# Kernel tuning notes

Hardware: AMD Instinct MI355X
Metric: run time of the kernel (lower is better)

## Reference

```python
import jax, jax.numpy as jnp
import numpy as np

N = 100_000        # nodes
E_HALF = 1_600_000 # undirected edges; symmetrized -> 3.2M directed
N_IN, N_HEMB, N_HGCN, N_OUT = 128, 32, 32, 1


def setup_inputs() -> dict:
    key = jax.random.key(0)
    ks = jax.random.split(key, 8)
    x = jax.random.normal(ks[0], (N, N_IN), dtype=jnp.float32)
    t = jax.random.uniform(ks[1], (N,), dtype=jnp.float32)
    # symmetric edge list (A = A^T), matching the typical undirected-graph usage
    src = jax.random.randint(ks[2], (E_HALF,), 0, N)
    dst = jax.random.randint(ks[3], (E_HALF,), 0, N)
    row = jnp.concatenate([src, dst]).astype(jnp.int32)
    col = jnp.concatenate([dst, src]).astype(jnp.int32)
    s = 0.05
    W_emb = jax.random.normal(ks[4], (N_IN, N_HEMB), jnp.float32) * s
    b_emb = jnp.zeros((N_HEMB,), jnp.float32)
    W_gcn = jax.random.normal(ks[5], (N_HEMB, N_HGCN), jnp.float32) * s
    b_gcn = jnp.zeros((N_HGCN,), jnp.float32)
    W1 = jax.random.normal(ks[6], (N_HGCN + 2, N_HEMB), jnp.float32) * s
    b1 = jnp.zeros((N_HEMB,), jnp.float32)
    W2 = jax.random.normal(ks[7], (N_HEMB, N_OUT), jnp.float32) * s
    b2 = jnp.zeros((N_OUT,), jnp.float32)
    return dict(x=x, t=t, row=row, col=col,
                W_emb=W_emb, b_emb=b_emb, W_gcn=W_gcn, b_gcn=b_gcn,
                W1=W1, b1=b1, W2=W2, b2=b2)


def reference(x, t, row, col, W_emb, b_emb, W_gcn, b_gcn, W1, b1, W2, b2):
    n = x.shape[0]
    h = jax.nn.relu(x @ W_emb + b_emb)                        # [N, Hemb]
    # per-edge attention score via gather + dot
    att = jnp.einsum('eh,eh->e', h[row], h[col])              # [E]
    att = jnp.exp(att - att.max())                            # global-max stabilized exp
    # per-node softmax denominator (segment sum over neighbors) + eps
    deno = jax.ops.segment_sum(att, row, num_segments=n) + 1e-8
    att = att / deno[row]                                     # normalized edge attention
    # exposure z: attention-weighted neighbor treatments
    z = jax.ops.segment_sum(att * t[col], row, num_segments=n)  # [N]
    # GCNConv (unit edge values: set_value() is non-inplace so adj_t stays valueless;
    # PyG then fills 1s, adds self loops, symmetric D^-1/2 norm)
    deg = jax.ops.segment_sum(jnp.ones(row.shape, jnp.float32), col, num_segments=n) + 1.0
    dis = jax.lax.rsqrt(deg)                                  # [N], deg >= 1
    hw = h @ W_gcn                                            # [N, Hgcn]
    msg = dis[row][:, None] * hw[row]                         # [E, Hgcn]
    agg = jax.ops.segment_sum(msg, col, num_segments=n)       # [N, Hgcn]
    gcn = dis[:, None] * agg + (dis * dis)[:, None] * hw + b_gcn
    rep = h + jax.nn.relu(gcn)                                # residual node rep
    feats = jnp.concatenate([rep, t[:, None], z[:, None]], axis=1)  # [N, Hgcn+2]
    out = jax.nn.relu(feats @ W1 + b1) @ W2 + b2              # [N, 1]
    return out, rep, z
```

## Files before the change

kernel.cpp:

```cpp
#include <hip/hip_runtime.h>
#include <hip/hip_bf16.h>
#include <hip/hip_fp16.h>

static constexpr int HN = 32;
static constexpr int NIN = 128;
static constexpr int CH1 = 8192;
static constexpr int CAP2 = 16384;

__device__ __forceinline__ float bf2f(unsigned short u) {
    union { unsigned int i; float f; } v;
    v.i = ((unsigned int)u) << 16;
    return v.f;
}
__device__ __forceinline__ float ldf(const void* p, size_t i, int isbf) {
    return isbf ? bf2f(((const unsigned short*)p)[i]) : ((const float*)p)[i];
}
__device__ __forceinline__ unsigned int pack2h(float a, float b) {
    unsigned short ua = __half_as_ushort(__float2half_rn(a));
    unsigned short ub = __half_as_ushort(__float2half_rn(b));
    return (unsigned int)ua | ((unsigned int)ub << 16);
}
__device__ __forceinline__ float2 up2(unsigned int u) {
    __half2 h2;
    *reinterpret_cast<unsigned int*>(&h2) = u;
    return __half22float2(h2);
}

__global__ void detect_kernel(const unsigned int* __restrict__ xw,
                              int* __restrict__ flag)
{
    int lane = threadIdx.x;
    int hits = 0;
    #pragma unroll
    for (int k = 0; k < 2; ++k) {
        unsigned int w = xw[lane + 64 * k];
        float a = bf2f((unsigned short)(w & 0xFFFFu));
        float aa = fabsf(a);
        if (a == 0.0f || (aa >= 0.000244140625f && aa <= 32.0f)) hits++;
    }
    #pragma unroll
    for (int m = 32; m; m >>= 1) hits += __shfl_xor(hits, m, 64);
    if (lane == 0) flag[0] = (hits >= 64) ? 1 : 0;
}

__global__ __launch_bounds__(256) void embed1_kernel(
    const void* __restrict__ x,
    const void* __restrict__ Wemb,
    const void* __restrict__ bemb,
    const int* __restrict__ flagp,
    float* __restrict__ h, int N)
{
    __shared__ float We[NIN * HN];
    __shared__ float be[HN];
    __shared__ float xs[32][NIN];
    const int tid = threadIdx.x;
    const int isbf = flagp[0];

    for (int i = tid; i < NIN * HN; i += 256) We[i] = ldf(Wemb, i, isbf);
    if (tid < HN) be[tid] = ldf(bemb, tid, isbf);

    const int n0 = blockIdx.x * 32;
    if (isbf) {
        const ushort4* x4 = (const ushort4*)((const unsigned short*)x + (size_t)n0 * NIN);
        for (int i = tid; i < 32 * (NIN / 4); i += 256) {
            ushort4 u = x4[i];
            int base = i * 4, n = base >> 7, k = base & (NIN - 1);
            xs[n][k] = bf2f(u.x); xs[n][k + 1] = bf2f(u.y);
            xs[n][k + 2] = bf2f(u.z); xs[n][k + 3] = bf2f(u.w);
        }
    } else {
        const float4* x4 = (const float4*)((const float*)x + (size_t)n0 * NIN);
        for (int i = tid; i < 32 * (NIN / 4); i += 256) {
            float4 u = x4[i];
            int base = i * 4, n = base >> 7, k = base & (NIN - 1);
            xs[n][k] = u.x; xs[n][k + 1] = u.y;
            xs[n][k + 2] = u.z; xs[n][k + 3] = u.w;
        }
    }
    __syncthreads();

    const int f = tid & 31, ns = tid >> 5;
    float a0 = be[f], a1 = be[f], a2 = be[f], a3 = be[f];
    #pragma unroll 8
    for (int k = 0; k < NIN; ++k) {
        float w = We[k * HN + f];
        a0 += xs[ns +  0][k] * w;
        a1 += xs[ns +  8][k] * w;
        a2 += xs[ns + 16][k] * w;
        a3 += xs[ns + 24][k] * w;
    }
    if (n0 + ns      < N) h[(size_t)(n0 + ns     ) * HN + f] = fmaxf(a0, 0.f);
    if (n0 + ns +  8 < N) h[(size_t)(n0 + ns +  8) * HN + f] = fmaxf(a1, 0.f);
    if (n0 + ns + 16 < N) h[(size_t)(n0 + ns + 16) * HN + f] = fmaxf(a2, 0.f);
    if (n0 + ns + 24 < N) h[(size_t)(n0 + ns + 24) * HN + f] = fmaxf(a3, 0.f);
}

__global__ __launch_bounds__(512) void bhist_kernel(
    const int* __restrict__ col, int* __restrict__ bucket_cnt, int E, int B)
{
    __shared__ int hist[512];
    const int t = threadIdx.x;
    const int e0 = blockIdx.x * CH1;
    for (int i = t; i < B; i += 512) hist[i] = 0;
    __syncthreads();
    #pragma unroll
    for (int k = 0; k < CH1 / 512; ++k) {
        int e = e0 + k * 512 + t;
        if (e < E) atomicAdd(&hist[col[e] >> 8], 1);
    }
    __syncthreads();
    for (int i = t; i < B; i += 512)
        if (hist[i]) atomicAdd(&bucket_cnt[i], hist[i]);
}

__global__ __launch_bounds__(512) void bscan_kernel(
    const int* __restrict__ bucket_cnt, int* __restrict__ bucket_base,
    int* __restrict__ bucket_cursor, int B, int E)
{
    __shared__ int sc[512];
    __shared__ int orig[512];
    const int t = threadIdx.x;
    int v0 = (t < B) ? bucket_cnt[t] : 0;
    sc[t] = v0; orig[t] = v0;
    __syncthreads();
    for (int o = 1; o < 512; o <<= 1) {
        int v = (t >= o) ? sc[t - o] : 0;
        __syncthreads();
        sc[t] += v;
        __syncthreads();
    }
    if (t < B) {
        int ex = sc[t] - orig[t];
        bucket_base[t] = ex;
        bucket_cursor[t] = ex;
    }
    if (t == 0) bucket_base[B] = E;
}

__global__ __launch_bounds__(512) void phase1_kernel(
    const int* __restrict__ row, const int* __restrict__ col,
    int* __restrict__ bucket_cursor, int* __restrict__ bucketed, int E, int B)
{
    __shared__ int hist[512];
    __shared__ int sc[512];
    __shared__ int cnt[512];
    __shared__ int gbase[512];
    __shared__ int word[CH1];
    __shared__ int dst[CH1];
    const int t = threadIdx.x;
    const int e0 = blockIdx.x * CH1;
    const int M = (E - e0 < CH1) ? (E - e0) : CH1;

    for (int i = t; i < B; i += 512) { hist[i] = 0; cnt[i] = 0; }
    __syncthreads();
    #pragma unroll
    for (int k = 0; k < CH1 / 512; ++k) {
        int e = e0 + k * 512 + t;
        if (e < E) atomicAdd(&hist[col[e] >> 8], 1);
    }
    __syncthreads();
    sc[t] = (t < B) ? hist[t] : 0;
    __syncthreads();
    for (int o = 1; o < 512; o <<= 1) {
        int v = (t >= o) ? sc[t - o] : 0;
        __syncthreads();
        sc[t] += v;
        __syncthreads();
    }
    if (t < B && hist[t])
        gbase[t] = atomicAdd(&bucket_cursor[t], hist[t]);
    __syncthreads();
    #pragma unroll
    for (int k = 0; k < CH1 / 512; ++k) {
        int e = e0 + k * 512 + t;
        if (e < E) {
            int c = col[e], r = row[e];
            int b = c >> 8;
            int lr = atomicAdd(&cnt[b], 1);
            int p = sc[b] - hist[b] + lr;
            word[p] = (r << 8) | (c & 255);
            dst[p] = gbase[b] + lr;
        }
    }
    __syncthreads();
    for (int i = t; i < M; i += 512)
        bucketed[dst[i]] = word[i];
}

__global__ __launch_bounds__(256) void phase2a_kernel(
    const int* __restrict__ bucketed, const int* __restrict__ bucket_base,
    int* __restrict__ count, int N)
{
    __shared__ int cnt[256];
    const int t = threadIdx.x, b = blockIdx.x;
    cnt[t] = 0;
    __syncthreads();
    const int s0 = bucket_base[b], s1 = bucket_base[b + 1];
    for (int i = s0 + t; i < s1; i += 256)
        atomicAdd(&cnt[bucketed[i] & 255], 1);
    __syncthreads();
    int node = (b << 8) + t;
    if (node < N) count[node] = cnt[t];
}

__global__ __launch_bounds__(256) void scan1_kernel(
    const int* __restrict__ count, int* __restrict__ bsum, int N)
{
    __shared__ int s[256];
    const int t = threadIdx.x, b = blockIdx.x;
    int base = b * 2048 + t * 8, sum = 0;
    #pragma unroll
    for (int k = 0; k < 8; ++k) { int i = base + k; if (i < N) sum += count[i]; }
    s[t] = sum; __syncthreads();
    for (int o = 128; o; o >>= 1) { if (t < o) s[t] += s[t + o]; __syncthreads(); }
    if (t == 0) bsum[b] = s[0];
}

__global__ void scan2_kernel(int* __restrict__ bsum, int nsb,
                             int* __restrict__ rowptr, int N, int E)
{
    if (threadIdx.x == 0 && blockIdx.x == 0) {
        int acc = 0;
        for (int i = 0; i < nsb; ++i) { int v = bsum[i]; bsum[i] = acc; acc += v; }
        rowptr[N] = E;
    }
}

__global__ __launch_bounds__(256) void scan3_kernel(
    int* __restrict__ countcur, const int* __restrict__ bsum,
    int* __restrict__ rowptr, int N)
{
    __shared__ int s[256];
    const int t = threadIdx.x, b = blockIdx.x;
    int base = b * 2048 + t * 8;
    int c[8]; int sum = 0;
    #pragma unroll
    for (int k = 0; k < 8; ++k) {
        int i = base + k;
        c[k] = (i < N) ? countcur[i] : 0;
        sum += c[k];
    }
    s[t] = sum; __syncthreads();
    for (int o = 1; o < 256; o <<= 1) {
        int v = (t >= o) ? s[t - o] : 0;
        __syncthreads();
        s[t] += v;
        __syncthreads();
    }
    int acc = bsum[b] + ((t == 0) ? 0 : s[t - 1]);
    #pragma unroll
    for (int k = 0; k < 8; ++k) {
        int i = base + k;
        if (i < N) { rowptr[i] = acc; countcur[i] = acc; acc += c[k]; }
    }
}

__global__ __launch_bounds__(256) void phase2b_kernel(
    const int* __restrict__ bucketed, const int* __restrict__ bucket_base,
    const int* __restrict__ rowptr, int* __restrict__ cursor,
    int* __restrict__ csr_src, int N)
{
    __shared__ int stage[CAP2];
    __shared__ int rps[257];
    __shared__ int cnt[256];
    const int t = threadIdx.x, b = blockIdx.x;
    const int s0 = bucket_base[b], s1 = bucket_base[b + 1];
    const int segsz = s1 - s0;
    const int node0 = b << 8;
    const int nodes = (N - node0 < 256) ? (N - node0) : 256;
    if (t <= nodes) rps[t] = rowptr[node0 + t];
    cnt[t] = 0;
    __syncthreads();
    if (segsz <= CAP2) {
        for (int i = s0 + t; i < s1; i += 256) {
            int w = bucketed[i];
            int lc = w & 255;
            int off = rps[lc] - s0 + atomicAdd(&cnt[lc], 1);
            stage[off] = w >> 8;
        }
        __syncthreads();
        for (int i = t; i < segsz; i += 256) csr_src[s0 + i] = stage[i];
    } else {
        for (int i = s0 + t; i < s1; i += 256) {
            int w = bucketed[i];
            int pos = atomicAdd(&cursor[node0 + (w & 255)], 1);
            csr_src[pos] = w >> 8;
        }
    }
}

__global__ __launch_bounds__(256) void embed2_kernel(
    const float* __restrict__ h, const void* __restrict__ Wgcn,
    const int* __restrict__ rowptr, const int* __restrict__ flagp,
    uint4* __restrict__ packed, int N)
{
    __shared__ float Wg[HN * HN];
    __shared__ float hs[32][HN + 1];
    __shared__ float ws[32][HN + 1];
    const int tid = threadIdx.x;
    const int isbf = flagp[0];
    for (int i = tid; i < HN * HN; i += 256) Wg[i] = ldf(Wgcn, i, isbf);
    const int n0 = blockIdx.x * 32;
    for (int i = tid; i < 32 * HN; i += 256) {
        int n = i >> 5, f = i & 31;
        hs[n][f] = (n0 + n < N) ? h[(size_t)(n0 + n) * HN + f] : 0.f;
    }
    __syncthreads();
    const int f = tid & 31, ns = tid >> 5;
    #pragma unroll
    for (int g = 0; g < 4; ++g) {
        int n = ns + 8 * g, v = n0 + n;
        float acc = 0.f;
        #pragma unroll
        for (int k = 0; k < HN; ++k) acc += hs[n][k] * Wg[k * HN + f];
        float dis = (v < N) ? rsqrtf((float)(rowptr[v + 1] - rowptr[v]) + 1.0f) : 0.f;
        ws[n][f] = dis * acc;
    }
    __syncthreads();
    const int n = tid >> 3, jj = tid & 7, v = n0 + n;
    if (v < N) {
        uint4 w;
        w.x = pack2h(hs[n][4 * jj + 0], hs[n][4 * jj + 1]);
        w.y = pack2h(hs[n][4 * jj + 2], hs[n][4 * jj + 3]);
        w.z = pack2h(ws[n][4 * jj + 0], ws[n][4 * jj + 1]);
        w.w = pack2h(ws[n][4 * jj + 2], ws[n][4 * jj + 3]);
        packed[(size_t)v * 8 + jj] = w;
    }
}

__global__ __launch_bounds__(256) void passB_kernel(
    const float* __restrict__ h, const uint4* __restrict__ packed,
    const int* __restrict__ csr_src, const int* __restrict__ rowptr,
    const void* __restrict__ t, const void* __restrict__ bgcn,
    const int* __restrict__ flagp,
    float* __restrict__ outr, float* __restrict__ outz,
    float* __restrict__ out0_ml, float* __restrict__ denout, int N)
{
    const int tid = threadIdx.x;
    const int lane = tid & 31;
    const int sub = lane >> 3;
    const int j = lane & 7;
    const int v = blockIdx.x * 8 + (tid >> 5);
    if (v >= N) return;
    const int isbf = flagp[0];

    const float4* h4 = (const float4*)h;
    float4 hv = h4[(size_t)v * 8 + j];
    uint4 sw = packed[(size_t)v * 8 + j];
    float2 wsv0 = up2(sw.z), wsv1 = up2(sw.w);
    const int s = rowptr[v], e2 = rowptr[v + 1];

    float m = -1e30f, den = 0.f, num = 0.f;
    float ax = 0.f, ay = 0.f, az = 0.f, aw = 0.f;
    int i = s + sub;
    for (; i + 4 < e2; i += 8) {
        int r0 = csr_src[i];
        int r1 = csr_src[i + 4];
        uint4 w0 = packed[(size_t)r0 * 8 + j];
        uint4 w1 = packed[(size_t)r1 * 8 + j];
        float tr0 = ldf(t, r0, isbf);
        float tr1 = ldf(t, r1, isbf);
        float2 h00 = up2(w0.x), h01 = up2(w0.y);
        float2 h10 = up2(w1.x), h11 = up2(w1.y);
        float p0 = hv.x * h00.x + hv.y * h00.y + hv.z * h01.x + hv.w * h01.y;
        float p1 = hv.x * h10.x + hv.y * h10.y + hv.z * h11.x + hv.w * h11.y;
        p0 += __shfl_xor(p0, 1, 32);
        p0 += __shfl_xor(p0, 2, 32);
        p0 += __shfl_xor(p0, 4, 32);
        p1 += __shfl_xor(p1, 1, 32);
        p1 += __shfl_xor(p1, 2, 32);
        p1 += __shfl_xor(p1, 4, 32);
        float2 a00 = up2(w0.z), a01 = up2(w0.w);
        float2 a10 = up2(w1.z), a11 = up2(w1.w);
        ax += a00.x + a10.x; ay += a00.y + a10.y;
        az += a01.x + a11.x; aw += a01.y + a11.y;
        float mn = fmaxf(m, fmaxf(p0, p1));
        float corr = __expf(m - mn);
        float e0 = __expf(p0 - mn), e1 = __expf(p1 - mn);
        den = den * corr + e0 + e1;
        num = num * corr + e0 * tr0 + e1 * tr1;
        m = mn;
    }
    if (i < e2) {
        int r0 = csr_src[i];
        uint4 w0 = packed[(size_t)r0 * 8 + j];
        float tr0 = ldf(t, r0, isbf);
        float2 h00 = up2(w0.x), h01 = up2(w0.y);
        float p0 = hv.x * h00.x + hv.y * h00.y + hv.z * h01.x + hv.w * h01.y;
        p0 += __shfl_xor(p0, 1, 32);
        p0 += __shfl_xor(p0, 2, 32);
        p0 += __shfl_xor(p0, 4, 32);
        float2 a00 = up2(w0.z), a01 = up2(w0.w);
        ax += a00.x; ay += a00.y; az += a01.x; aw += a01.y;
        float mn = fmaxf(m, p0);
        float corr = __expf(m - mn);
        float e0 = __expf(p0 - mn);
        den = den * corr + e0;
        num = num * corr + e0 * tr0;
        m = mn;
    }
    #pragma unroll
    for (int o = 8; o <= 16; o <<= 1) {
        float mo = __shfl_xor(m, o, 32);
        float dno = __shfl_xor(den, o, 32);
        float nmo = __shfl_xor(num, o, 32);
        float mn = fmaxf(m, mo);
        float ca = __expf(m - mn), cb = __expf(mo - mn);
        den = den * ca + dno * cb;
        num = num * ca + nmo * cb;
        m = mn;
        ax += __shfl_xor(ax, o, 32);
        ay += __shfl_xor(ay, o, 32);
        az += __shfl_xor(az, o, 32);
        aw += __shfl_xor(aw, o, 32);
    }

    float dv = rsqrtf((float)(e2 - s) + 1.0f);
    float4 rep;
    rep.x = hv.x + fmaxf(dv * (ax + wsv0.x) + ldf(bgcn, 4 * j + 0, isbf), 0.f);
    rep.y = hv.y + fmaxf(dv * (ay + wsv0.y) + ldf(bgcn, 4 * j + 1, isbf), 0.f);
    rep.z = hv.z + fmaxf(dv * (az + wsv1.x) + ldf(bgcn, 4 * j + 2, isbf), 0.f);
    rep.w = hv.w + fmaxf(dv * (aw + wsv1.y) + ldf(bgcn, 4 * j + 3, isbf), 0.f);
    if (sub == 0)
        ((float4*)outr)[(size_t)v * 8 + j] = rep;
    if (lane == 0) {
        outz[v]    = num / fmaxf(den, 1e-37f);
        out0_ml[v] = m;
        denout[v]  = den;
    }
}

__global__ __launch_bounds__(256) void amax1_kernel(
    const float* __restrict__ ml, float* __restrict__ bmax2, int N)
{
    float m = -INFINITY;
    for (int i = blockIdx.x * 256 + threadIdx.x; i < N; i += 256 * 256)
        m = fmaxf(m, ml[i]);
    #pragma unroll
    for (int s = 32; s; s >>= 1) m = fmaxf(m, __shfl_xor(m, s, 64));
    __shared__ float sm[4];
    if ((threadIdx.x & 63) == 0) sm[threadIdx.x >> 6] = m;
    __syncthreads();
    if (threadIdx.x == 0)
        bmax2[blockIdx.x] = fmaxf(fmaxf(sm[0], sm[1]), fmaxf(sm[2], sm[3]));
}
__global__ __launch_bounds__(256) void amax2_kernel(
    const float* __restrict__ bmax2, float* __restrict__ amax)
{
    float m = bmax2[threadIdx.x];
    #pragma unroll
    for (int s = 32; s; s >>= 1) m = fmaxf(m, __shfl_xor(m, s, 64));
    __shared__ float sm[4];
    if ((threadIdx.x & 63) == 0) sm[threadIdx.x >> 6] = m;
    __syncthreads();
    if (threadIdx.x == 0) amax[0] = fmaxf(fmaxf(sm[0], sm[1]), fmaxf(sm[2], sm[3]));
}

__global__ __launch_bounds__(256) void final_kernel(
    const float* __restrict__ rep_in,
    const void* __restrict__ t, const int* __restrict__ flagp,
    const float* __restrict__ amax, const float* __restrict__ denarr,
    const void* __restrict__ W1, const void* __restrict__ b1,
    const void* __restrict__ W2, const void* __restrict__ b2,
    float* __restrict__ out0, float* __restrict__ outz, int N)
{
    __shared__ float W1s[34 * HN];
    __shared__ float b1s[HN], W2s[HN];
    __shared__ float b2s;
    const int tid = threadIdx.x;
    const int isbf = flagp[0];
    for (int i = tid; i < 34 * HN; i += 256) W1s[i] = ldf(W1, i, isbf);
    if (tid < HN) {
        b1s[tid] = ldf(b1, tid, isbf);
        W2s[tid] = ldf(W2, tid, isbf);
    }
    if (tid == 0) b2s = ldf(b2, 0, isbf);
    __syncthreads();

    const int lane = tid & 31;
    const int v = blockIdx.x * 8 + (tid >> 5);
    if (v >= N) return;

    float rep = rep_in[(size_t)v * HN + lane];
    float ml  = out0[v];
    float den = denarr[v];
    float zh  = outz[v];
    float am  = amax[0];
    float term = (1e-8f / den) * expf(am - ml);
    float z = zh / (1.0f + term);
    float tv = ldf(t, v, isbf);

    float acc = b1s[lane] + tv * W1s[32 * HN + lane] + z * W1s[33 * HN + lane];
    #pragma unroll
    for (int k = 0; k < HN; ++k)
        acc += __shfl(rep, k, 32) * W1s[k * HN + lane];
    float f1 = fmaxf(acc, 0.f);
    float o = f1 * W2s[lane];
    #pragma unroll
    for (int m = 16; m; m >>= 1) o += __shfl_xor(o, m, 32);

    if (lane == 0) {
        out0[v] = o + b2s;
        outz[v] = z;
    }
}

extern "C" void kernel_launch(void* const* d_in, const int* in_sizes, int n_in,
                              void* d_out, int out_size, void* d_ws, size_t ws_size,
                              hipStream_t stream)
{
    const int N = out_size / 34;
    const int E = in_sizes[2];

    const void* x    = d_in[0];
    const void* t    = d_in[1];
    const int* row   = (const int*)d_in[2];
    const int* col   = (const int*)d_in[3];
    const void* Wemb = d_in[4];
    const void* bemb = d_in[5];
    const void* Wgcn = d_in[6];
    const void* bgcn = d_in[7];
    const void* W1   = d_in[8];
    const void* b1   = d_in[9];
    const void* W2   = d_in[10];
    const void* b2   = d_in[11];

    const int B   = (N + 255) >> 8;
    const int nsb = (N + 2047) / 2048;
    const int NB1 = (E + CH1 - 1) / CH1;

    char* wsb = (char*)d_ws;
    size_t off = 0;
    float* h        = (float*)(wsb + off); off += (size_t)N * HN * 4;
    size_t hwbytes  = (size_t)N * HN * 4;
    if ((size_t)E * 4 > hwbytes) hwbytes = (size_t)E * 4;
    char*  hwreg    = wsb + off;           off += hwbytes;
    int*   csr_src  = (int*)(wsb + off);   off += (size_t)E * 4;
    int*   rowptr   = (int*)(wsb + off);   off += (size_t)(N + 1) * 4;
    int*   count    = (int*)(wsb + off);   off += (size_t)N * 4;
    int*   bucket_cnt    = (int*)(wsb + off); off += (size_t)B * 4;
    int*   bucket_base   = (int*)(wsb + off); off += (size_t)(B + 1) * 4;
    int*   bucket_cursor = (int*)(wsb + off); off += (size_t)B * 4;
    float* bmax2    = (float*)(wsb + off); off += 256 * 4;
    int*   bsum     = (int*)(wsb + off);   off += (size_t)nsb * 4;
    float* amax     = (float*)(wsb + off); off += 4;
    int*   flag     = (int*)(wsb + off);   off += 4;

    int*   bucketed = (int*)hwreg;
    uint4* packed   = (uint4*)hwreg;

    hipMemsetAsync(bucket_cnt, 0, (size_t)B * 4, stream);

    detect_kernel<<<1, 64, 0, stream>>>((const unsigned int*)x, flag);
    embed1_kernel<<<(N + 31) / 32, 256, 0, stream>>>(x, Wemb, bemb, flag, h, N);

    bhist_kernel<<<NB1, 512, 0, stream>>>(col, bucket_cnt, E, B);
    bscan_kernel<<<1, 512, 0, stream>>>(bucket_cnt, bucket_base,
                                        bucket_cursor, B, E);
    phase1_kernel<<<NB1, 512, 0, stream>>>(row, col, bucket_cursor,
                                           bucketed, E, B);
    phase2a_kernel<<<B, 256, 0, stream>>>(bucketed, bucket_base, count, N);
    scan1_kernel<<<nsb, 256, 0, stream>>>(count, bsum, N);
    scan2_kernel<<<1, 64, 0, stream>>>(bsum, nsb, rowptr, N, E);
    scan3_kernel<<<nsb, 256, 0, stream>>>(count, bsum, rowptr, N);
    phase2b_kernel<<<B, 256, 0, stream>>>(bucketed, bucket_base, rowptr,
                                          count, csr_src, N);
    embed2_kernel<<<(N + 31) / 32, 256, 0, stream>>>(h, Wgcn, rowptr, flag,
                                                     packed, N);

    float* outp = (float*)d_out;
    float* out0 = outp;
    float* outr = outp + N;
    float* outz = outp + (size_t)N * 33;
    float* den  = (float*)count;

    passB_kernel<<<(N + 7) / 8, 256, 0, stream>>>(
        h, packed, csr_src, rowptr, t, bgcn, flag, outr, outz, out0, den, N);
    amax1_kernel<<<256, 256, 0, stream>>>(out0, bmax2, N);
    amax2_kernel<<<1, 256, 0, stream>>>(bmax2, amax);
    final_kernel<<<(N + 7) / 8, 256, 0, stream>>>(
        outr, t, flag, amax, den, W1, b1, W2, b2, out0, outz, N);
}
```

Before: 357.2 us.

## Build CSR from global per-node degree count, dropping bucket histogram passes

```diff
diff --git a/kernel.cpp b/kernel.cpp
--- a/kernel.cpp
+++ b/kernel.cpp
@@ -4,8 +4,9 @@
 
 static constexpr int HN = 32;
 static constexpr int NIN = 128;
-static constexpr int CH1 = 8192;
+static constexpr int CH1 = 4096;
 static constexpr int CAP2 = 16384;
+static constexpr float LOG2E = 1.4426950408889634f;
 
 __device__ __forceinline__ float bf2f(unsigned short u) {
     union { unsigned int i; float f; } v;
@@ -95,46 +96,12 @@
     if (n0 + ns + 24 < N) h[(size_t)(n0 + ns + 24) * HN + f] = fmaxf(a3, 0.f);
 }
 
-__global__ __launch_bounds__(512) void bhist_kernel(
-    const int* __restrict__ col, int* __restrict__ bucket_cnt, int E, int B)
-{
-    __shared__ int hist[512];
-    const int t = threadIdx.x;
-    const int e0 = blockIdx.x * CH1;
-    for (int i = t; i < B; i += 512) hist[i] = 0;
-    __syncthreads();
-    #pragma unroll
-    for (int k = 0; k < CH1 / 512; ++k) {
-        int e = e0 + k * 512 + t;
-        if (e < E) atomicAdd(&hist[col[e] >> 8], 1);
-    }
-    __syncthreads();
-    for (int i = t; i < B; i += 512)
-        if (hist[i]) atomicAdd(&bucket_cnt[i], hist[i]);
-}
-
-__global__ __launch_bounds__(512) void bscan_kernel(
-    const int* __restrict__ bucket_cnt, int* __restrict__ bucket_base,
-    int* __restrict__ bucket_cursor, int B, int E)
-{
-    __shared__ int sc[512];
-    __shared__ int orig[512];
-    const int t = threadIdx.x;
-    int v0 = (t < B) ? bucket_cnt[t] : 0;
-    sc[t] = v0; orig[t] = v0;
-    __syncthreads();
-    for (int o = 1; o < 512; o <<= 1) {
-        int v = (t >= o) ? sc[t - o] : 0;
-        __syncthreads();
-        sc[t] += v;
-        __syncthreads();
-    }
-    if (t < B) {
-        int ex = sc[t] - orig[t];
-        bucket_base[t] = ex;
-        bucket_cursor[t] = ex;
-    }
-    if (t == 0) bucket_base[B] = E;
+__global__ __launch_bounds__(256) void degcnt_kernel(
+    const int* __restrict__ col, int* __restrict__ count, int E)
+{
+    const int stride = gridDim.x * 256;
+    for (int i = blockIdx.x * 256 + threadIdx.x; i < E; i += stride)
+        atomicAdd(&count[col[i]], 1);
 }
 
 __global__ __launch_bounds__(512) void phase1_kernel(
@@ -187,22 +154,6 @@
         bucketed[dst[i]] = word[i];
 }
 
-__global__ __launch_bounds__(256) void phase2a_kernel(
-    const int* __restrict__ bucketed, const int* __restrict__ bucket_base,
-    int* __restrict__ count, int N)
-{
-    __shared__ int cnt[256];
-    const int t = threadIdx.x, b = blockIdx.x;
-    cnt[t] = 0;
-    __syncthreads();
-    const int s0 = bucket_base[b], s1 = bucket_base[b + 1];
-    for (int i = s0 + t; i < s1; i += 256)
-        atomicAdd(&cnt[bucketed[i] & 255], 1);
-    __syncthreads();
-    int node = (b << 8) + t;
-    if (node < N) count[node] = cnt[t];
-}
-
 __global__ __launch_bounds__(256) void scan1_kernel(
     const int* __restrict__ count, int* __restrict__ bsum, int N)
 {
@@ -219,16 +170,26 @@
 __global__ void scan2_kernel(int* __restrict__ bsum, int nsb,
                              int* __restrict__ rowptr, int N, int E)
 {
-    if (threadIdx.x == 0 && blockIdx.x == 0) {
+    const int lane = threadIdx.x;
+    if (nsb <= 64) {
+        int v = (lane < nsb) ? bsum[lane] : 0;
+        int s = v;
+        #pragma unroll
+        for (int o = 1; o < 64; o <<= 1) {
+            int u = __shfl_up(s, o, 64);
+            if (lane >= o) s += u;
+        }
+        if (lane < nsb) bsum[lane] = s - v;
+    } else if (lane == 0) {
         int acc = 0;
         for (int i = 0; i < nsb; ++i) { int v = bsum[i]; bsum[i] = acc; acc += v; }
-        rowptr[N] = E;
-    }
+    }
+    if (lane == 0) rowptr[N] = E;
 }
 
 __global__ __launch_bounds__(256) void scan3_kernel(
     int* __restrict__ countcur, const int* __restrict__ bsum,
-    int* __restrict__ rowptr, int N)
+    int* __restrict__ rowptr, int* __restrict__ bucket_cursor, int N)
 {
     __shared__ int s[256];
     const int t = threadIdx.x, b = blockIdx.x;
@@ -251,12 +212,17 @@
     #pragma unroll
     for (int k = 0; k < 8; ++k) {
         int i = base + k;
-        if (i < N) { rowptr[i] = acc; countcur[i] = acc; acc += c[k]; }
+        if (i < N) {
+            rowptr[i] = acc;
+            countcur[i] = acc;
+            if ((i & 255) == 0) bucket_cursor[i >> 8] = acc;
+            acc += c[k];
+        }
     }
 }
 
 __global__ __launch_bounds__(256) void phase2b_kernel(
-    const int* __restrict__ bucketed, const int* __restrict__ bucket_base,
+    const int* __restrict__ bucketed,
     const int* __restrict__ rowptr, int* __restrict__ cursor,
     int* __restrict__ csr_src, int N)
 {
@@ -264,13 +230,13 @@
     __shared__ int rps[257];
     __shared__ int cnt[256];
     const int t = threadIdx.x, b = blockIdx.x;
-    const int s0 = bucket_base[b], s1 = bucket_base[b + 1];
-    const int segsz = s1 - s0;
     const int node0 = b << 8;
     const int nodes = (N - node0 < 256) ? (N - node0) : 256;
-    if (t <= nodes) rps[t] = rowptr[node0 + t];
+    for (int i = t; i <= nodes; i += 256) rps[i] = rowptr[node0 + i];
     cnt[t] = 0;
     __syncthreads();
+    const int s0 = rps[0], s1 = rps[nodes];
+    const int segsz = s1 - s0;
     if (segsz <= CAP2) {
         for (int i = s0 + t; i < s1; i += 256) {
             int w = bucketed[i];
@@ -370,13 +336,14 @@
         p1 += __shfl_xor(p1, 1, 32);
         p1 += __shfl_xor(p1, 2, 32);
         p1 += __shfl_xor(p1, 4, 32);
+        p0 *= LOG2E; p1 *= LOG2E;
         float2 a00 = up2(w0.z), a01 = up2(w0.w);
         float2 a10 = up2(w1.z), a11 = up2(w1.w);
         ax += a00.x + a10.x; ay += a00.y + a10.y;
         az += a01.x + a11.x; aw += a01.y + a11.y;
         float mn = fmaxf(m, fmaxf(p0, p1));
-        float corr = __expf(m - mn);
-        float e0 = __expf(p0 - mn), e1 = __expf(p1 - mn);
+        float corr = exp2f(m - mn);
+        float e0 = exp2f(p0 - mn), e1 = exp2f(p1 - mn);
         den = den * corr + e0 + e1;
         num = num * corr + e0 * tr0 + e1 * tr1;
         m = mn;
@@ -390,11 +357,12 @@
         p0 += __shfl_xor(p0, 1, 32);
         p0 += __shfl_xor(p0, 2, 32);
         p0 += __shfl_xor(p0, 4, 32);
+        p0 *= LOG2E;
         float2 a00 = up2(w0.z), a01 = up2(w0.w);
         ax += a00.x; ay += a00.y; az += a01.x; aw += a01.y;
         float mn = fmaxf(m, p0);
-        float corr = __expf(m - mn);
-        float e0 = __expf(p0 - mn);
+        float corr = exp2f(m - mn);
+        float e0 = exp2f(p0 - mn);
         den = den * corr + e0;
         num = num * corr + e0 * tr0;
         m = mn;
@@ -405,7 +373,7 @@
         float dno = __shfl_xor(den, o, 32);
         float nmo = __shfl_xor(num, o, 32);
         float mn = fmaxf(m, mo);
-        float ca = __expf(m - mn), cb = __expf(mo - mn);
+        float ca = exp2f(m - mn), cb = exp2f(mo - mn);
         den = den * ca + dno * cb;
         num = num * ca + nmo * cb;
         m = mn;
@@ -486,7 +454,7 @@
     float den = denarr[v];
     float zh  = outz[v];
     float am  = amax[0];
-    float term = (1e-8f / den) * expf(am - ml);
+    float term = (1e-8f / den) * exp2f(am - ml);
     float z = zh / (1.0f + term);
     float tv = ldf(t, v, isbf);
 
@@ -538,8 +506,6 @@
     int*   csr_src  = (int*)(wsb + off);   off += (size_t)E * 4;
     int*   rowptr   = (int*)(wsb + off);   off += (size_t)(N + 1) * 4;
     int*   count    = (int*)(wsb + off);   off += (size_t)N * 4;
-    int*   bucket_cnt    = (int*)(wsb + off); off += (size_t)B * 4;
-    int*   bucket_base   = (int*)(wsb + off); off += (size_t)(B + 1) * 4;
     int*   bucket_cursor = (int*)(wsb + off); off += (size_t)B * 4;
     float* bmax2    = (float*)(wsb + off); off += 256 * 4;
     int*   bsum     = (int*)(wsb + off);   off += (size_t)nsb * 4;
@@ -549,22 +515,18 @@
     int*   bucketed = (int*)hwreg;
     uint4* packed   = (uint4*)hwreg;
 
-    hipMemsetAsync(bucket_cnt, 0, (size_t)B * 4, stream);
+    hipMemsetAsync(count, 0, (size_t)N * 4, stream);
 
     detect_kernel<<<1, 64, 0, stream>>>((const unsigned int*)x, flag);
     embed1_kernel<<<(N + 31) / 32, 256, 0, stream>>>(x, Wemb, bemb, flag, h, N);
 
-    bhist_kernel<<<NB1, 512, 0, stream>>>(col, bucket_cnt, E, B);
-    bscan_kernel<<<1, 512, 0, stream>>>(bucket_cnt, bucket_base,
-                                        bucket_cursor, B, E);
+    degcnt_kernel<<<2048, 256, 0, stream>>>(col, count, E);
+    scan1_kernel<<<nsb, 256, 0, stream>>>(count, bsum, N);
+    scan2_kernel<<<1, 64, 0, stream>>>(bsum, nsb, rowptr, N, E);
+    scan3_kernel<<<nsb, 256, 0, stream>>>(count, bsum, rowptr, bucket_cursor, N);
     phase1_kernel<<<NB1, 512, 0, stream>>>(row, col, bucket_cursor,
                                            bucketed, E, B);
-    phase2a_kernel<<<B, 256, 0, stream>>>(bucketed, bucket_base, count, N);
-    scan1_kernel<<<nsb, 256, 0, stream>>>(count, bsum, N);
-    scan2_kernel<<<1, 64, 0, stream>>>(bsum, nsb, rowptr, N, E);
-    scan3_kernel<<<nsb, 256, 0, stream>>>(count, bsum, rowptr, N);
-    phase2b_kernel<<<B, 256, 0, stream>>>(bucketed, bucket_base, rowptr,
-                                          count, csr_src, N);
+    phase2b_kernel<<<B, 256, 0, stream>>>(bucketed, rowptr, count, csr_src, N);
     embed2_kernel<<<(N + 31) / 32, 256, 0, stream>>>(h, Wgcn, rowptr, flag,
                                                      packed, N);
 
```

Measured after the change: 468.6 us. 1.31x slower.

## Fuse CSR count, scan and scatter into one per-bucket kernel; use exp2

Applied to the files above, without the earlier changes.

```diff
diff --git a/kernel.cpp b/kernel.cpp
--- a/kernel.cpp
+++ b/kernel.cpp
@@ -6,6 +6,7 @@
 static constexpr int NIN = 128;
 static constexpr int CH1 = 8192;
 static constexpr int CAP2 = 16384;
+static constexpr float LOG2E = 1.4426950408889634f;
 
 __device__ __forceinline__ float bf2f(unsigned short u) {
     union { unsigned int i; float f; } v;
@@ -115,7 +116,8 @@
 
 __global__ __launch_bounds__(512) void bscan_kernel(
     const int* __restrict__ bucket_cnt, int* __restrict__ bucket_base,
-    int* __restrict__ bucket_cursor, int B, int E)
+    int* __restrict__ bucket_cursor, int* __restrict__ rowptr,
+    int B, int N, int E)
 {
     __shared__ int sc[512];
     __shared__ int orig[512];
@@ -134,7 +136,7 @@
         bucket_base[t] = ex;
         bucket_cursor[t] = ex;
     }
-    if (t == 0) bucket_base[B] = E;
+    if (t == 0) { bucket_base[B] = E; rowptr[N] = E; }
 }
 
 __global__ __launch_bounds__(512) void phase1_kernel(
@@ -187,95 +189,42 @@
         bucketed[dst[i]] = word[i];
 }
 
-__global__ __launch_bounds__(256) void phase2a_kernel(
+__global__ __launch_bounds__(256) void phase2_kernel(
     const int* __restrict__ bucketed, const int* __restrict__ bucket_base,
-    int* __restrict__ count, int N)
-{
+    int* __restrict__ rowptr, int* __restrict__ csr_src, int N)
+{
+    __shared__ int stage[CAP2];
     __shared__ int cnt[256];
+    __shared__ int sc[256];
+    __shared__ int loc[256];
     const int t = threadIdx.x, b = blockIdx.x;
+    const int node0 = b << 8;
+    const int s0 = bucket_base[b], s1 = bucket_base[b + 1];
+    const int segsz = s1 - s0;
     cnt[t] = 0;
     __syncthreads();
-    const int s0 = bucket_base[b], s1 = bucket_base[b + 1];
     for (int i = s0 + t; i < s1; i += 256)
         atomicAdd(&cnt[bucketed[i] & 255], 1);
     __syncthreads();
-    int node = (b << 8) + t;
-    if (node < N) count[node] = cnt[t];
-}
-
-__global__ __launch_bounds__(256) void scan1_kernel(
-    const int* __restrict__ count, int* __restrict__ bsum, int N)
-{
-    __shared__ int s[256];
-    const int t = threadIdx.x, b = blockIdx.x;
-    int base = b * 2048 + t * 8, sum = 0;
-    #pragma unroll
-    for (int k = 0; k < 8; ++k) { int i = base + k; if (i < N) sum += count[i]; }
-    s[t] = sum; __syncthreads();
-    for (int o = 128; o; o >>= 1) { if (t < o) s[t] += s[t + o]; __syncthreads(); }
-    if (t == 0) bsum[b] = s[0];
-}
-
-__global__ void scan2_kernel(int* __restrict__ bsum, int nsb,
-                             int* __restrict__ rowptr, int N, int E)
-{
-    if (threadIdx.x == 0 && blockIdx.x == 0) {
-        int acc = 0;
-        for (int i = 0; i < nsb; ++i) { int v = bsum[i]; bsum[i] = acc; acc += v; }
-        rowptr[N] = E;
-    }
-}
-
-__global__ __launch_bounds__(256) void scan3_kernel(
-    int* __restrict__ countcur, const int* __restrict__ bsum,
-    int* __restrict__ rowptr, int N)
-{
-    __shared__ int s[256];
-    const int t = threadIdx.x, b = blockIdx.x;
-    int base = b * 2048 + t * 8;
-    int c[8]; int sum = 0;
-    #pragma unroll
-    for (int k = 0; k < 8; ++k) {
-        int i = base + k;
-        c[k] = (i < N) ? countcur[i] : 0;
-        sum += c[k];
-    }
-    s[t] = sum; __syncthreads();
+    int c = cnt[t];
+    sc[t] = c;
+    __syncthreads();
     for (int o = 1; o < 256; o <<= 1) {
-        int v = (t >= o) ? s[t - o] : 0;
-        __syncthreads();
-        s[t] += v;
-        __syncthreads();
-    }
-    int acc = bsum[b] + ((t == 0) ? 0 : s[t - 1]);
-    #pragma unroll
-    for (int k = 0; k < 8; ++k) {
-        int i = base + k;
-        if (i < N) { rowptr[i] = acc; countcur[i] = acc; acc += c[k]; }
-    }
-}
-
-__global__ __launch_bounds__(256) void phase2b_kernel(
-    const int* __restrict__ bucketed, const int* __restrict__ bucket_base,
-    const int* __restrict__ rowptr, int* __restrict__ cursor,
-    int* __restrict__ csr_src, int N)
-{
-    __shared__ int stage[CAP2];
-    __shared__ int rps[257];
-    __shared__ int cnt[256];
-    const int t = threadIdx.x, b = blockIdx.x;
-    const int s0 = bucket_base[b], s1 = bucket_base[b + 1];
-    const int segsz = s1 - s0;
-    const int node0 = b << 8;
-    const int nodes = (N - node0 < 256) ? (N - node0) : 256;
-    if (t <= nodes) rps[t] = rowptr[node0 + t];
+        int v = (t >= o) ? sc[t - o] : 0;
+        __syncthreads();
+        sc[t] += v;
+        __syncthreads();
+    }
+    int ex = sc[t] - c;
+    loc[t] = ex;
+    if (node0 + t < N) rowptr[node0 + t] = s0 + ex;
     cnt[t] = 0;
     __syncthreads();
     if (segsz <= CAP2) {
         for (int i = s0 + t; i < s1; i += 256) {
             int w = bucketed[i];
             int lc = w & 255;
-            int off = rps[lc] - s0 + atomicAdd(&cnt[lc], 1);
+            int off = loc[lc] + atomicAdd(&cnt[lc], 1);
             stage[off] = w >> 8;
         }
         __syncthreads();
@@ -283,8 +232,9 @@
     } else {
         for (int i = s0 + t; i < s1; i += 256) {
             int w = bucketed[i];
-            int pos = atomicAdd(&cursor[node0 + (w & 255)], 1);
-            csr_src[pos] = w >> 8;
+            int lc = w & 255;
+            int off = loc[lc] + atomicAdd(&cnt[lc], 1);
+            csr_src[s0 + off] = w >> 8;
         }
     }
 }
@@ -370,13 +320,14 @@
         p1 += __shfl_xor(p1, 1, 32);
         p1 += __shfl_xor(p1, 2, 32);
         p1 += __shfl_xor(p1, 4, 32);
+        p0 *= LOG2E; p1 *= LOG2E;
         float2 a00 = up2(w0.z), a01 = up2(w0.w);
         float2 a10 = up2(w1.z), a11 = up2(w1.w);
         ax += a00.x + a10.x; ay += a00.y + a10.y;
         az += a01.x + a11.x; aw += a01.y + a11.y;
         float mn = fmaxf(m, fmaxf(p0, p1));
-        float corr = __expf(m - mn);
-        float e0 = __expf(p0 - mn), e1 = __expf(p1 - mn);
+        float corr = exp2f(m - mn);
+        float e0 = exp2f(p0 - mn), e1 = exp2f(p1 - mn);
         den = den * corr + e0 + e1;
         num = num * corr + e0 * tr0 + e1 * tr1;
         m = mn;
@@ -390,11 +341,12 @@
         p0 += __shfl_xor(p0, 1, 32);
         p0 += __shfl_xor(p0, 2, 32);
         p0 += __shfl_xor(p0, 4, 32);
+        p0 *= LOG2E;
         float2 a00 = up2(w0.z), a01 = up2(w0.w);
         ax += a00.x; ay += a00.y; az += a01.x; aw += a01.y;
         float mn = fmaxf(m, p0);
-        float corr = __expf(m - mn);
-        float e0 = __expf(p0 - mn);
+        float corr = exp2f(m - mn);
+        float e0 = exp2f(p0 - mn);
         den = den * corr + e0;
         num = num * corr + e0 * tr0;
         m = mn;
@@ -405,7 +357,7 @@
         float dno = __shfl_xor(den, o, 32);
         float nmo = __shfl_xor(num, o, 32);
         float mn = fmaxf(m, mo);
-        float ca = __expf(m - mn), cb = __expf(mo - mn);
+        float ca = exp2f(m - mn), cb = exp2f(mo - mn);
         den = den * ca + dno * cb;
         num = num * ca + nmo * cb;
         m = mn;
@@ -486,7 +438,7 @@
     float den = denarr[v];
     float zh  = outz[v];
     float am  = amax[0];
-    float term = (1e-8f / den) * expf(am - ml);
+    float term = (1e-8f / den) * exp2f(am - ml);
     float z = zh / (1.0f + term);
     float tv = ldf(t, v, isbf);
 
@@ -526,7 +478,6 @@
     const void* b2   = d_in[11];
 
     const int B   = (N + 255) >> 8;
-    const int nsb = (N + 2047) / 2048;
     const int NB1 = (E + CH1 - 1) / CH1;
 
     char* wsb = (char*)d_ws;
@@ -537,12 +488,11 @@
     char*  hwreg    = wsb + off;           off += hwbytes;
     int*   csr_src  = (int*)(wsb + off);   off += (size_t)E * 4;
     int*   rowptr   = (int*)(wsb + off);   off += (size_t)(N + 1) * 4;
-    int*   count    = (int*)(wsb + off);   off += (size_t)N * 4;
+    float* den      = (float*)(wsb + off); off += (size_t)N * 4;
     int*   bucket_cnt    = (int*)(wsb + off); off += (size_t)B * 4;
     int*   bucket_base   = (int*)(wsb + off); off += (size_t)(B + 1) * 4;
     int*   bucket_cursor = (int*)(wsb + off); off += (size_t)B * 4;
     float* bmax2    = (float*)(wsb + off); off += 256 * 4;
-    int*   bsum     = (int*)(wsb + off);   off += (size_t)nsb * 4;
     float* amax     = (float*)(wsb + off); off += 4;
     int*   flag     = (int*)(wsb + off);   off += 4;
 
@@ -556,15 +506,11 @@
 
     bhist_kernel<<<NB1, 512, 0, stream>>>(col, bucket_cnt, E, B);
     bscan_kernel<<<1, 512, 0, stream>>>(bucket_cnt, bucket_base,
-                                        bucket_cursor, B, E);
+                                        bucket_cursor, rowptr, B, N, E);
     phase1_kernel<<<NB1, 512, 0, stream>>>(row, col, bucket_cursor,
                                            bucketed, E, B);
-    phase2a_kernel<<<B, 256, 0, stream>>>(bucketed, bucket_base, count, N);
-    scan1_kernel<<<nsb, 256, 0, stream>>>(count, bsum, N);
-    scan2_kernel<<<1, 64, 0, stream>>>(bsum, nsb, rowptr, N, E);
-    scan3_kernel<<<nsb, 256, 0, stream>>>(count, bsum, rowptr, N);
-    phase2b_kernel<<<B, 256, 0, stream>>>(bucketed, bucket_base, rowptr,
-                                          count, csr_src, N);
+    phase2_kernel<<<B, 256, 0, stream>>>(bucketed, bucket_base, rowptr,
+                                         csr_src, N);
     embed2_kernel<<<(N + 31) / 32, 256, 0, stream>>>(h, Wgcn, rowptr, flag,
                                                      packed, N);
 
@@ -572,7 +518,6 @@
     float* out0 = outp;
     float* outr = outp + N;
     float* outz = outp + (size_t)N * 33;
-    float* den  = (float*)count;
 
     passB_kernel<<<(N + 7) / 8, 256, 0, stream>>>(
         h, packed, csr_src, rowptr, t, bgcn, flag, outr, outz, out0, den, N);
```

Measured after the change: 340.7 us. 1.05x faster.
